# Kernel tuning notes

Measured on AMD Instinct MI355X. Metric: run time of the kernel, lower is better.

## Reference

```python
import jax, jax.numpy as jnp
import numpy as np

NUM_COLS = 8      # MyTopoAgent.num_columns
NUM_SELECTED = 4  # MyTopoAgent.num_selected


def _gatv2(x, src, tgt, Wl, bl, Wr, br, att, bias, n):
    """PyG GATv2Conv (share_weights=False, concat=True, negative_slope=0.2).
    x: [n, Din]; src/tgt: [E] (self loops already appended); att: [H, C]."""
    H, C = att.shape
    xl = (x @ Wl + bl).reshape(n, H, C)   # lin_l(x) -> source transform
    xr = (x @ Wr + br).reshape(n, H, C)   # lin_r(x) -> target transform
    # e_ij = att . leaky_relu(xl[j] + xr[i])  per head
    e = jnp.einsum('ehc,hc->eh', jax.nn.leaky_relu(xl[src] + xr[tgt], 0.2), att)  # [E, H]
    # segment softmax over edges sharing a target node (stable via segment max)
    m = jax.lax.stop_gradient(jax.ops.segment_max(e, tgt, num_segments=n))
    ex = jnp.exp(e - m[tgt])
    denom = jax.ops.segment_sum(ex, tgt, num_segments=n)
    alpha = ex / (denom[tgt] + 1e-16)
    out = jax.ops.segment_sum(xl[src] * alpha[..., None], tgt, num_segments=n)  # [n, H, C]
    return out.reshape(n, H * C) + bias


def setup_inputs() -> dict:
    key = jax.random.key(0)
    B, N, D, Hd, Ch, E = 4, 10000, 128, 128, 7, 640000
    M = B * N
    ks = iter(jax.random.split(key, 40))
    nx = lambda shape: jax.random.normal(next(ks), shape, dtype=jnp.float32) * 0.05
    inp = {}
    inp['x'] = jax.random.normal(next(ks), (B, N, D), dtype=jnp.float32)
    inp['edge_index'] = jax.random.randint(next(ks), (2, E), 0, M)
    inp['gumbel_u'] = jax.random.uniform(next(ks), (B, NUM_COLS, Ch), dtype=jnp.float32,
                                         minval=1e-6, maxval=1.0 - 1e-6)
    # actor gat1(D->Hd), actor gat2(Hd->Ch), critic gat1(D->Hd), critic gat2(Hd->Hd); heads=1
    for pre, di, do in (('a1', D, Hd), ('a2', Hd, Ch), ('c1', D, Hd), ('c2', Hd, Hd)):
        inp[pre + '_Wl'] = nx((di, do))
        inp[pre + '_bl'] = jnp.zeros((do,), jnp.float32)
        inp[pre + '_Wr'] = nx((di, do))
        inp[pre + '_br'] = jnp.zeros((do,), jnp.float32)
        inp[pre + '_att'] = nx((1, do))
        inp[pre + '_b'] = jnp.zeros((do,), jnp.float32)
    inp['fc_W'] = nx((Hd, 1))
    inp['fc_b'] = jnp.zeros((1,), jnp.float32)
    return inp


def reference(x, edge_index, gumbel_u,
              a1_Wl, a1_bl, a1_Wr, a1_br, a1_att, a1_b,
              a2_Wl, a2_bl, a2_Wr, a2_br, a2_att, a2_b,
              c1_Wl, c1_bl, c1_Wr, c1_br, c1_att, c1_b,
              c2_Wl, c2_bl, c2_Wr, c2_br, c2_att, c2_b,
              fc_W, fc_b):
    B, N, D = x.shape
    M = B * N
    xf = x.reshape(M, D)
    loops = jnp.arange(M, dtype=edge_index.dtype)  # PyG add_self_loops
    src = jnp.concatenate([edge_index[0], loops])
    tgt = jnp.concatenate([edge_index[1], loops])
    # ---- actor: GATv2 -> leaky_relu(0.01) -> GATv2 -> softmax ----
    h = _gatv2(xf, src, tgt, a1_Wl, a1_bl, a1_Wr, a1_br, a1_att, a1_b, M)
    h = jax.nn.leaky_relu(h, 0.01)
    logits = _gatv2(h, src, tgt, a2_Wl, a2_bl, a2_Wr, a2_br, a2_att, a2_b, M).reshape(B, N, -1)
    probs = jax.nn.softmax(logits, axis=-1)  # [B, N, 7]
    # multinomial(k=4, no replacement) per column via Gumbel top-k
    g = -jnp.log(-jnp.log(gumbel_u))                       # [B, 8, 7]
    scores = jnp.log(probs[:, :NUM_COLS, :]) + g
    _, action = jax.lax.top_k(scores, NUM_SELECTED)        # [B, 8, 4]
    # torch gather(dim=1): sel[b,i,j] = probs[b, action[b,i,j], j]
    sel = probs[jnp.arange(B)[:, None, None], action, jnp.arange(NUM_SELECTED)[None, None, :]]
    # ---- critic: GATv2 -> leaky_relu(0.01) -> GATv2 -> Linear ----
    hc = _gatv2(xf, src, tgt, c1_Wl, c1_bl, c1_Wr, c1_br, c1_att, c1_b, M)
    hc = jax.nn.leaky_relu(hc, 0.01)
    hc = _gatv2(hc, src, tgt, c2_Wl, c2_bl, c2_Wr, c2_br, c2_att, c2_b, M).reshape(B, N, -1)
    value = hc @ fc_W + fc_b  # [B, N, 1]
    return action, sel, value
```

## Files before the change

kernel.cpp:

```cpp
#include <hip/hip_runtime.h>
#include <math.h>


typedef __attribute__((ext_vector_type(8))) short bf16x8;
typedef __attribute__((ext_vector_type(4))) float f32x4;

__device__ __forceinline__ float wave_reduce_sum(float v){
  #pragma unroll
  for (int o = 32; o > 0; o >>= 1) v += __shfl_xor(v, o);
  return v;
}
__device__ __forceinline__ unsigned short f2bf(float f){
  unsigned int u = __float_as_uint(f);
  u += 0x7FFFu + ((u >> 16) & 1u);
  return (unsigned short)(u >> 16);
}
__device__ __forceinline__ void unpack2(unsigned int u, float& a, float& b){
  a = __uint_as_float(u << 16);
  b = __uint_as_float(u & 0xffff0000u);
}

__global__ void k_scatter(const int* __restrict__ ei, int E,
                          int* __restrict__ cnt, int* __restrict__ bucket,
                          const float* __restrict__ W1l, const float* __restrict__ W1r,
                          const float* __restrict__ W2l, const float* __restrict__ W2r,
                          unsigned short* __restrict__ Wt1, unsigned short* __restrict__ Wt2){
  int e = blockIdx.x * blockDim.x + threadIdx.x;
  if (e < E){
    int s = ei[e], t = ei[E + e];
    int pos = atomicAdd(&cnt[t], 1);
    if (pos < 64) bucket[(size_t)t * 64 + pos] = s;
  } else {
    int r = e - E;
    if (r < 65536){
      int which = r >> 15;
      int lin = r & 32767;
      const float* Wl = which ? W2l : W1l;
      const float* Wr = which ? W2r : W1r;
      unsigned short* Wt = which ? Wt2 : Wt1;
      int n = lin >> 7, k = lin & 127;
      float v = (n < 128) ? Wl[(size_t)k * 128 + n] : Wr[(size_t)k * 128 + (n - 128)];
      Wt[lin] = f2bf(v);
    }
  }
}

__global__ void k_mark1(const int* __restrict__ cnt, const int* __restrict__ bucket,
                        int* __restrict__ flag1, int* __restrict__ list1,
                        int* __restrict__ n1, int N){
  int p = threadIdx.x;
  if (p >= 32) return;
  int node = (p >> 3) * N + (p & 7);
  if (atomicExch(&flag1[node], 1) == 0) list1[atomicAdd(n1, 1)] = node;
  int deg = min(cnt[node], 64);
  const int* crow = bucket + (size_t)node * 64;
  for (int j = 0; j < deg; ++j){
    int s = crow[j];
    if (atomicExch(&flag1[s], 1) == 0) list1[atomicAdd(n1, 1)] = s;
  }
}
__global__ void k_mark2(const int* __restrict__ cnt, const int* __restrict__ bucket,
                        const int* __restrict__ list1, const int* __restrict__ n1,
                        int* __restrict__ flag2, int* __restrict__ list2,
                        int* __restrict__ n2){
  int n = *n1;
  for (int i = blockIdx.x * blockDim.x + threadIdx.x; i < n; i += gridDim.x * blockDim.x){
    int node = list1[i];
    if (atomicExch(&flag2[node], 1) == 0) list2[atomicAdd(n2, 1)] = node;
    int deg = min(cnt[node], 64);
    const int* crow = bucket + (size_t)node * 64;
    for (int j = 0; j < deg; ++j){
      int s = crow[j];
      if (atomicExch(&flag2[s], 1) == 0) list2[atomicAdd(n2, 1)] = s;
    }
  }
}

__device__ __forceinline__ void dev_gemm_dual(
    int bid, const float* __restrict__ A,
    const float* __restrict__ Wl, const float* __restrict__ Wr,
    const float* __restrict__ blv, const float* __restrict__ brv,
    float* __restrict__ XL1, float* __restrict__ XR1,
    const int* __restrict__ list1, const int* __restrict__ list2,
    const int* __restrict__ nn,
    float (*As)[17], float (*Ws)[64]){
  int side = bid >> 7;
  int rem = bid & 127;
  const float* W = side ? Wr : Wl;
  const float* bias = side ? brv : blv;
  float* Out = side ? XR1 : XL1;
  const int* rows = side ? list1 : list2;
  int n = side ? nn[0] : nn[1];
  int tid = threadIdx.x;
  int tx = tid & 15, ty = tid >> 4;
  int colBase = (rem >> 6) * 64;
  int bx = rem & 63;
  int ar = tid >> 2, ac = (tid & 3) << 2;
  int kr = tid >> 4, nc = (tid & 15) << 2;
  for (int base = bx * 64; base < n; base += 64 * 64){
    float acc[4][4] = {};
    int arow = rows[min(base + ar, n - 1)];
    for (int k0 = 0; k0 < 128; k0 += 16){
      float4 av = *(const float4*)(A + (size_t)arow * 128 + k0 + ac);
      As[ar][ac + 0] = av.x; As[ar][ac + 1] = av.y;
      As[ar][ac + 2] = av.z; As[ar][ac + 3] = av.w;
      float4 wv = *(const float4*)(W + (size_t)(k0 + kr) * 128 + colBase + nc);
      *(float4*)&Ws[kr][nc] = wv;
      __syncthreads();
      #pragma unroll
      for (int kk = 0; kk < 16; ++kk){
        float a0 = As[ty * 4 + 0][kk];
        float a1 = As[ty * 4 + 1][kk];
        float a2 = As[ty * 4 + 2][kk];
        float a3 = As[ty * 4 + 3][kk];
        float4 b = *(const float4*)&Ws[kk][tx * 4];
        acc[0][0] += a0 * b.x; acc[0][1] += a0 * b.y; acc[0][2] += a0 * b.z; acc[0][3] += a0 * b.w;
        acc[1][0] += a1 * b.x; acc[1][1] += a1 * b.y; acc[1][2] += a1 * b.z; acc[1][3] += a1 * b.w;
        acc[2][0] += a2 * b.x; acc[2][1] += a2 * b.y; acc[2][2] += a2 * b.z; acc[2][3] += a2 * b.w;
        acc[3][0] += a3 * b.x; acc[3][1] += a3 * b.y; acc[3][2] += a3 * b.z; acc[3][3] += a3 * b.w;
      }
      __syncthreads();
    }
    int cN = colBase + tx * 4;
    float4 bb = *(const float4*)(bias + cN);
    #pragma unroll
    for (int i = 0; i < 4; ++i){
      int r = rows[min(base + ty * 4 + i, n - 1)];
      float4 o;
      o.x = acc[i][0] + bb.x; o.y = acc[i][1] + bb.y;
      o.z = acc[i][2] + bb.z; o.w = acc[i][3] + bb.w;
      *(float4*)(Out + (size_t)r * 128 + cN) = o;
    }
  }
}

template<bool CVT>
__device__ __forceinline__ void dev_gemm_mfma(
    int rblk, const void* __restrict__ Av, const unsigned short* __restrict__ Wt,
    const float* __restrict__ bl, const float* __restrict__ br,
    unsigned short* __restrict__ XL, unsigned short* __restrict__ XR){
  int w = threadIdx.x >> 6, lane = threadIdx.x & 63;
  int l16 = lane & 15, kg = lane >> 4;
  int rBase = rblk * 64 + w * 16;
  f32x4 acc[16];
  #pragma unroll
  for (int i = 0; i < 16; ++i) acc[i] = (f32x4){0.f, 0.f, 0.f, 0.f};
  #pragma unroll
  for (int ks = 0; ks < 4; ++ks){
    bf16x8 a;
    if constexpr (CVT){
      const float* A = (const float*)Av;
      const float* ap = A + (size_t)(rBase + l16) * 128 + ks * 32 + kg * 8;
      float4 f0 = *(const float4*)ap;
      float4 f1 = *(const float4*)(ap + 4);
      union { bf16x8 v; unsigned short s[8]; } u;
      u.s[0] = f2bf(f0.x); u.s[1] = f2bf(f0.y); u.s[2] = f2bf(f0.z); u.s[3] = f2bf(f0.w);
      u.s[4] = f2bf(f1.x); u.s[5] = f2bf(f1.y); u.s[6] = f2bf(f1.z); u.s[7] = f2bf(f1.w);
      a = u.v;
    } else {
      a = *(const bf16x8*)((const unsigned short*)Av + (size_t)(rBase + l16) * 128 + ks * 32 + kg * 8);
    }
    #pragma unroll
    for (int ct = 0; ct < 16; ++ct){
      bf16x8 wv = *(const bf16x8*)(Wt + (size_t)(ct * 16 + l16) * 128 + ks * 32 + kg * 8);
      acc[ct] = __builtin_amdgcn_mfma_f32_16x16x32_bf16(wv, a, acc[ct], 0, 0, 0);
    }
  }
  int row = rBase + l16;
  #pragma unroll
  for (int ct = 0; ct < 16; ++ct){
    int col = ct * 16 + kg * 4;
    const float* bp = (col < 128) ? (bl + col) : (br + (col - 128));
    float4 bb = *(const float4*)bp;
    unsigned int p0 = (unsigned int)f2bf(acc[ct][0] + bb.x) |
                      ((unsigned int)f2bf(acc[ct][1] + bb.y) << 16);
    unsigned int p1 = (unsigned int)f2bf(acc[ct][2] + bb.z) |
                      ((unsigned int)f2bf(acc[ct][3] + bb.w) << 16);
    unsigned short* dst = (col < 128) ? (XL + (size_t)row * 128 + col)
                                      : (XR + (size_t)row * 128 + (col - 128));
    uint2 pk; pk.x = p0; pk.y = p1;
    *(uint2*)dst = pk;
  }
}

template<int MODE>
__device__ __forceinline__ void dev_gather16(
    int gid, int l,
    const unsigned short* __restrict__ XL, const unsigned short* __restrict__ XR,
    const int* __restrict__ cnt, const int* __restrict__ bucket,
    const float* __restrict__ att, const float* __restrict__ bias,
    const float* __restrict__ fcW, const float* __restrict__ fcb,
    void* __restrict__ outp){
  uint4 xu = *(const uint4*)(XR + (size_t)gid * 128 + l * 8);
  float xr[8];
  unpack2(xu.x, xr[0], xr[1]); unpack2(xu.y, xr[2], xr[3]);
  unpack2(xu.z, xr[4], xr[5]); unpack2(xu.w, xr[6], xr[7]);
  float at[8];
  {
    float4 a0 = *(const float4*)(att + l * 8);
    float4 a1 = *(const float4*)(att + l * 8 + 4);
    at[0] = a0.x; at[1] = a0.y; at[2] = a0.z; at[3] = a0.w;
    at[4] = a1.x; at[5] = a1.y; at[6] = a1.z; at[7] = a1.w;
  }
  int deg = min(cnt[gid], 64);
  const int* __restrict__ crow = bucket + (size_t)gid * 64;
  float m = -INFINITY, den = 0.f;
  float acc[8] = {0.f, 0.f, 0.f, 0.f, 0.f, 0.f, 0.f, 0.f};

  auto proc = [&](uint4 u){
    float xl[8];
    unpack2(u.x, xl[0], xl[1]); unpack2(u.y, xl[2], xl[3]);
    unpack2(u.z, xl[4], xl[5]); unpack2(u.w, xl[6], xl[7]);
    float e = 0.f;
    #pragma unroll
    for (int c = 0; c < 8; ++c){
      float v = xl[c] + xr[c];
      v = fmaxf(v, 0.2f * v);
      e = fmaf(v, at[c], e);
    }
    e += __shfl_xor(e, 1, 16);
    e += __shfl_xor(e, 2, 16);
    e += __shfl_xor(e, 4, 16);
    e += __shfl_xor(e, 8, 16);
    if (e > m){
      float sc = __expf(m - e);
      den *= sc;
      #pragma unroll
      for (int c = 0; c < 8; ++c) acc[c] *= sc;
      m = e;
    }
    float p = __expf(e - m);
    den += p;
    #pragma unroll
    for (int c = 0; c < 8; ++c) acc[c] = fmaf(p, xl[c], acc[c]);
  };

  proc(*(const uint4*)(XL + (size_t)gid * 128 + l * 8));

  int nq = deg >> 2;
  int j = 0;
  if (nq > 0){
    uint4 r0, r1, r2, r3;
    {
      int s0 = crow[0], s1 = crow[1], s2 = crow[2], s3 = crow[3];
      r0 = *(const uint4*)(XL + (size_t)s0 * 128 + l * 8);
      r1 = *(const uint4*)(XL + (size_t)s1 * 128 + l * 8);
      r2 = *(const uint4*)(XL + (size_t)s2 * 128 + l * 8);
      r3 = *(const uint4*)(XL + (size_t)s3 * 128 + l * 8);
    }
    for (int q = 1;; ++q){
      bool more = (q < nq);
      uint4 n0, n1, n2, n3;
      if (more){
        int b4 = q * 4;
        int t0 = crow[b4 + 0], t1 = crow[b4 + 1], t2 = crow[b4 + 2], t3 = crow[b4 + 3];
        n0 = *(const uint4*)(XL + (size_t)t0 * 128 + l * 8);
        n1 = *(const uint4*)(XL + (size_t)t1 * 128 + l * 8);
        n2 = *(const uint4*)(XL + (size_t)t2 * 128 + l * 8);
        n3 = *(const uint4*)(XL + (size_t)t3 * 128 + l * 8);
      }
      proc(r0); proc(r1); proc(r2); proc(r3);
      if (!more) break;
      r0 = n0; r1 = n1; r2 = n2; r3 = n3;
    }
    j = nq * 4;
  }
  for (; j < deg; ++j){
    int s = crow[j];
    proc(*(const uint4*)(XL + (size_t)s * 128 + l * 8));
  }

  float r = 1.f / (den + 1e-16f);
  float4 b0 = *(const float4*)(bias + l * 8);
  float4 b1 = *(const float4*)(bias + l * 8 + 4);
  float o[8];
  o[0] = acc[0] * r + b0.x; o[1] = acc[1] * r + b0.y;
  o[2] = acc[2] * r + b0.z; o[3] = acc[3] * r + b0.w;
  o[4] = acc[4] * r + b1.x; o[5] = acc[5] * r + b1.y;
  o[6] = acc[6] * r + b1.z; o[7] = acc[7] * r + b1.w;
  if (MODE == 0){
    #pragma unroll
    for (int c = 0; c < 8; ++c) o[c] = o[c] > 0.f ? o[c] : 0.01f * o[c];
    uint4 pk;
    pk.x = (unsigned int)f2bf(o[0]) | ((unsigned int)f2bf(o[1]) << 16);
    pk.y = (unsigned int)f2bf(o[2]) | ((unsigned int)f2bf(o[3]) << 16);
    pk.z = (unsigned int)f2bf(o[4]) | ((unsigned int)f2bf(o[5]) << 16);
    pk.w = (unsigned int)f2bf(o[6]) | ((unsigned int)f2bf(o[7]) << 16);
    *(uint4*)((unsigned short*)outp + (size_t)gid * 128 + l * 8) = pk;
  } else {
    float4 w0 = *(const float4*)(fcW + l * 8);
    float4 w1 = *(const float4*)(fcW + l * 8 + 4);
    float pv = o[0] * w0.x + o[1] * w0.y + o[2] * w0.z + o[3] * w0.w +
               o[4] * w1.x + o[5] * w1.y + o[6] * w1.z + o[7] * w1.w;
    pv += __shfl_xor(pv, 1, 16);
    pv += __shfl_xor(pv, 2, 16);
    pv += __shfl_xor(pv, 4, 16);
    pv += __shfl_xor(pv, 8, 16);
    if (l == 0) ((float*)outp)[gid] = pv + fcb[0];
  }
}

__device__ __forceinline__ void dev_a1_fused(
    int vbid,
    const float* __restrict__ XL, const float* __restrict__ XR,
    const int* __restrict__ cnt, const int* __restrict__ bucket,
    const float* __restrict__ att, const float* __restrict__ bias,
    const float* __restrict__ Wl7, const float* __restrict__ Wr7,
    const float* __restrict__ bl7, const float* __restrict__ br7,
    float* __restrict__ XL2, float* __restrict__ XR2,
    const int* __restrict__ list, const int* __restrict__ n_dev){
  int n = *n_dev;
  int lane = threadIdx.x & 63;
  const int wstride = (256 * 256) >> 6;
  for (int i = (vbid * 256 + (int)threadIdx.x) >> 6; i < n; i += wstride){
    int wid = list[i];
    float2 xr = ((const float2*)(XR + (size_t)wid * 128))[lane];
    float2 at = ((const float2*)att)[lane];
    int deg = min(cnt[wid], 64);
    const int* crow = bucket + (size_t)wid * 64;
    float m = -INFINITY, den = 0.f, acc0 = 0.f, acc1 = 0.f;
    for (int j = -1; j < deg; ++j){
      int s = (j < 0) ? wid : crow[j];
      float2 xl = ((const float2*)(XL + (size_t)s * 128))[lane];
      float v0 = xl.x + xr.x, v1 = xl.y + xr.y;
      v0 = v0 > 0.f ? v0 : 0.2f * v0;
      v1 = v1 > 0.f ? v1 : 0.2f * v1;
      float e = wave_reduce_sum(v0 * at.x + v1 * at.y);
      float mn = fmaxf(m, e);
      float sc = __expf(m - mn);
      float p  = __expf(e - mn);
      den  = den  * sc + p;
      acc0 = acc0 * sc + p * xl.x;
      acc1 = acc1 * sc + p * xl.y;
      m = mn;
    }
    float r = 1.f / (den + 1e-16f);
    float2 bs = ((const float2*)bias)[lane];
    float o0 = acc0 * r + bs.x;
    float o1 = acc1 * r + bs.y;
    o0 = o0 > 0.f ? o0 : 0.01f * o0;
    o1 = o1 > 0.f ? o1 : 0.01f * o1;
    #pragma unroll
    for (int c = 0; c < 7; ++c){
      float wl0 = Wl7[(size_t)(2 * lane) * 7 + c];
      float wl1 = Wl7[(size_t)(2 * lane + 1) * 7 + c];
      float wr0 = Wr7[(size_t)(2 * lane) * 7 + c];
      float wr1 = Wr7[(size_t)(2 * lane + 1) * 7 + c];
      float dl = wave_reduce_sum(o0 * wl0 + o1 * wl1);
      float dr = wave_reduce_sum(o0 * wr0 + o1 * wr1);
      if (lane == 0){
        XL2[(size_t)wid * 8 + c] = dl + bl7[c];
        XR2[(size_t)wid * 8 + c] = dr + br7[c];
      }
    }
  }
}

__device__ __forceinline__ void dev_a2head(
    float (*pr)[8],
    const float* __restrict__ XL2, const float* __restrict__ XR2,
    const int* __restrict__ cnt, const int* __restrict__ bucket,
    const float* __restrict__ att, const float* __restrict__ bias,
    const float* __restrict__ gu,
    float* __restrict__ out_action, float* __restrict__ out_sel, int N){
  int g = threadIdx.x >> 3, c = threadIdx.x & 7;
  int node = (g >> 3) * N + (g & 7);
  float xr = (c < 7) ? XR2[(size_t)node * 8 + c] : 0.f;
  float at = (c < 7) ? att[c] : 0.f;
  int deg = min(cnt[node], 64);
  const int* crow = bucket + (size_t)node * 64;
  float m = -INFINITY, den = 0.f, acc = 0.f;
  for (int j = -1; j < deg; ++j){
    int s = (j < 0) ? node : crow[j];
    float xl = (c < 7) ? XL2[(size_t)s * 8 + c] : 0.f;
    float v = xl + xr;
    v = fmaxf(v, 0.2f * v);
    float e = v * at;
    e += __shfl_xor(e, 1, 8);
    e += __shfl_xor(e, 2, 8);
    e += __shfl_xor(e, 4, 8);
    if (e > m){
      float sc = __expf(m - e);
      den *= sc; acc *= sc; m = e;
    }
    float p = __expf(e - m);
    den += p;
    acc = fmaf(p, xl, acc);
  }
  float lg = acc / (den + 1e-16f) + ((c < 7) ? bias[c] : 0.f);
  float lgv = (c < 7) ? lg : -INFINITY;
  float mx = lgv;
  mx = fmaxf(mx, __shfl_xor(mx, 1, 8));
  mx = fmaxf(mx, __shfl_xor(mx, 2, 8));
  mx = fmaxf(mx, __shfl_xor(mx, 4, 8));
  float ex = (c < 7) ? expf(lgv - mx) : 0.f;
  float sm = ex;
  sm += __shfl_xor(sm, 1, 8);
  sm += __shfl_xor(sm, 2, 8);
  sm += __shfl_xor(sm, 4, 8);
  pr[g][c] = ex / sm;
  __syncthreads();
  int t = threadIdx.x;
  if (t < 32){
    int b = t >> 3;
    float sc[7];
    #pragma unroll
    for (int cc = 0; cc < 7; ++cc){
      float u = gu[t * 7 + cc];
      float gn = -logf(-logf(u));
      sc[cc] = logf(pr[t][cc]) + gn;
    }
    #pragma unroll
    for (int k = 0; k < 4; ++k){
      float best = -INFINITY; int bi = 0;
      #pragma unroll
      for (int cc = 0; cc < 7; ++cc) if (sc[cc] > best){ best = sc[cc]; bi = cc; }
      sc[bi] = -INFINITY;
      out_action[t * 4 + k] = (float)bi;
      out_sel[t * 4 + k] = pr[b * 8 + bi][k];
    }
  }
}

__global__ __launch_bounds__(256) void k_mega1(
    const float* __restrict__ x,
    const float* __restrict__ a1_Wl, const float* __restrict__ a1_Wr,
    const float* __restrict__ a1_bl, const float* __restrict__ a1_br,
    float* __restrict__ XL1, float* __restrict__ XR1,
    const int* __restrict__ list1, const int* __restrict__ list2,
    const int* __restrict__ nn,
    const unsigned short* __restrict__ Wt1,
    const float* __restrict__ c1_bl, const float* __restrict__ c1_br,
    unsigned short* __restrict__ XLb, unsigned short* __restrict__ XRb){
  __shared__ float As[64][17];
  __shared__ float Ws[16][64];
  int bid = blockIdx.x;
  if (bid < 256){
    dev_gemm_dual(bid, x, a1_Wl, a1_Wr, a1_bl, a1_br, XL1, XR1, list1, list2, nn, As, Ws);
  } else {
    dev_gemm_mfma<true>(bid - 256, x, Wt1, c1_bl, c1_br, XLb, XRb);
  }
}

__global__ __launch_bounds__(256) void k_mega2(
    const unsigned short* __restrict__ XLb, const unsigned short* __restrict__ XRb,
    const int* __restrict__ cnt, const int* __restrict__ bucket,
    const float* __restrict__ c1_att, const float* __restrict__ c1_b,
    unsigned short* __restrict__ Hb, int M, int G0,
    const float* __restrict__ XL1, const float* __restrict__ XR1,
    const float* __restrict__ a1_att, const float* __restrict__ a1_b,
    const float* __restrict__ Wl7, const float* __restrict__ Wr7,
    const float* __restrict__ bl7, const float* __restrict__ br7,
    float* __restrict__ XL2, float* __restrict__ XR2,
    const int* __restrict__ list1, const int* __restrict__ n1){
  int bid = blockIdx.x;
  if (bid < G0){
    int gid = (bid * 256 + (int)threadIdx.x) >> 4;
    int l = threadIdx.x & 15;
    if (gid < M)
      dev_gather16<0>(gid, l, XLb, XRb, cnt, bucket, c1_att, c1_b,
                      nullptr, nullptr, (void*)Hb);
  } else {
    dev_a1_fused(bid - G0, XL1, XR1, cnt, bucket, a1_att, a1_b,
                 Wl7, Wr7, bl7, br7, XL2, XR2, list1, n1);
  }
}

__global__ __launch_bounds__(256) void k_mega3(
    const unsigned short* __restrict__ Hb, const unsigned short* __restrict__ Wt2,
    const float* __restrict__ c2_bl, const float* __restrict__ c2_br,
    unsigned short* __restrict__ XLb, unsigned short* __restrict__ XRb, int nMfma,
    const float* __restrict__ XL2, const float* __restrict__ XR2,
    const int* __restrict__ cnt, const int* __restrict__ bucket,
    const float* __restrict__ a2_att, const float* __restrict__ a2_b,
    const float* __restrict__ gu,
    float* __restrict__ out_action, float* __restrict__ out_sel, int N){
  __shared__ float pr[32][8];
  int bid = blockIdx.x;
  if (bid < nMfma){
    dev_gemm_mfma<false>(bid, Hb, Wt2, c2_bl, c2_br, XLb, XRb);
  } else {
    dev_a2head(pr, XL2, XR2, cnt, bucket, a2_att, a2_b, gu, out_action, out_sel, N);
  }
}

__global__ __launch_bounds__(256) void k_gather_v(
    const unsigned short* __restrict__ XLb, const unsigned short* __restrict__ XRb,
    const int* __restrict__ cnt, const int* __restrict__ bucket,
    const float* __restrict__ att, const float* __restrict__ bias,
    const float* __restrict__ fcW, const float* __restrict__ fcb,
    float* __restrict__ out_value, int M){
  int gid = (blockIdx.x * blockDim.x + threadIdx.x) >> 4;
  int l = threadIdx.x & 15;
  if (gid < M)
    dev_gather16<1>(gid, l, XLb, XRb, cnt, bucket, att, bias, fcW, fcb, (void*)out_value);
}

extern "C" void kernel_launch(void* const* d_in, const int* in_sizes, int n_in,
                              void* d_out, int out_size, void* d_ws, size_t ws_size,
                              hipStream_t stream){
  const float* x  = (const float*)d_in[0];
  const int*   ei = (const int*)d_in[1];
  const float* gu = (const float*)d_in[2];
  const float* a1_Wl = (const float*)d_in[3],  *a1_bl = (const float*)d_in[4];
  const float* a1_Wr = (const float*)d_in[5],  *a1_br = (const float*)d_in[6];
  const float* a1_att= (const float*)d_in[7],  *a1_b  = (const float*)d_in[8];
  const float* a2_Wl = (const float*)d_in[9],  *a2_bl = (const float*)d_in[10];
  const float* a2_Wr = (const float*)d_in[11], *a2_br = (const float*)d_in[12];
  const float* a2_att= (const float*)d_in[13], *a2_b  = (const float*)d_in[14];
  const float* c1_Wl = (const float*)d_in[15], *c1_bl = (const float*)d_in[16];
  const float* c1_Wr = (const float*)d_in[17], *c1_br = (const float*)d_in[18];
  const float* c1_att= (const float*)d_in[19], *c1_b  = (const float*)d_in[20];
  const float* c2_Wl = (const float*)d_in[21], *c2_bl = (const float*)d_in[22];
  const float* c2_Wr = (const float*)d_in[23], *c2_br = (const float*)d_in[24];
  const float* c2_att= (const float*)d_in[25], *c2_b  = (const float*)d_in[26];
  const float* fc_W  = (const float*)d_in[27], *fc_b  = (const float*)d_in[28];

  const int M = in_sizes[0] / 128;
  const int E = in_sizes[1] / 2;
  const int B = in_sizes[2] / 56;
  const int N = M / B;
  const int nw = B * 8;
  const int T = 256;

  char* ws = (char*)d_ws;
  size_t off = 0;
  auto alloc = [&](size_t bytes) -> void* {
    void* p = ws + off;
    off += (bytes + 255) & ~(size_t)255;
    return p;
  };
  int*   cnt    = (int*)alloc((size_t)(3 * M + 2) * 4);
  int*   flag1  = cnt + M;
  int*   flag2  = flag1 + M;
  int*   nn     = flag2 + M;
  int*   bucket = (int*)alloc((size_t)M * 64 * 4);
  int*   list1  = (int*)alloc((size_t)M * 4);
  int*   list2  = (int*)alloc((size_t)M * 4);
  float* XL2    = (float*)alloc((size_t)M * 8 * 4);
  float* XR2    = (float*)alloc((size_t)M * 8 * 4);
  unsigned short* Wt1 = (unsigned short*)alloc((size_t)256 * 128 * 2);
  unsigned short* Wt2 = (unsigned short*)alloc((size_t)256 * 128 * 2);
  float* XL1 = (float*)alloc((size_t)M * 128 * 4);
  float* XR1 = (float*)alloc((size_t)M * 128 * 4);
  unsigned short* XLb = (unsigned short*)alloc((size_t)M * 128 * 2);
  unsigned short* XRb = (unsigned short*)alloc((size_t)M * 128 * 2);
  unsigned short* Hb  = (unsigned short*)alloc((size_t)M * 128 * 2);
  (void)ws_size; (void)n_in; (void)out_size;

  float* out_action = (float*)d_out;
  float* out_sel    = out_action + (size_t)nw * 4;
  float* out_value  = out_sel + (size_t)nw * 4;

  const int G0 = (M * 16 + T - 1) / T;
  const int nMfma = M / 64;

  hipMemsetAsync(cnt, 0, (size_t)(3 * M + 2) * 4, stream);
  k_scatter<<<(E + 65536 + T - 1) / T, T, 0, stream>>>(ei, E, cnt, bucket,
      c1_Wl, c1_Wr, c2_Wl, c2_Wr, Wt1, Wt2);

  k_mark1<<<1, 64, 0, stream>>>(cnt, bucket, flag1, list1, &nn[0], N);
  k_mark2<<<64, T, 0, stream>>>(cnt, bucket, list1, &nn[0], flag2, list2, &nn[1]);

  k_mega1<<<256 + nMfma, T, 0, stream>>>(x, a1_Wl, a1_Wr, a1_bl, a1_br,
      XL1, XR1, list1, list2, nn, Wt1, c1_bl, c1_br, XLb, XRb);

  k_mega2<<<G0 + 256, T, 0, stream>>>(XLb, XRb, cnt, bucket, c1_att, c1_b,
      Hb, M, G0, XL1, XR1, a1_att, a1_b, a2_Wl, a2_Wr, a2_bl, a2_br,
      XL2, XR2, list1, &nn[0]);

  k_mega3<<<nMfma + 1, T, 0, stream>>>(Hb, Wt2, c2_bl, c2_br, XLb, XRb, nMfma,
      XL2, XR2, cnt, bucket, a2_att, a2_b, gu, out_action, out_sel, N);

  k_gather_v<<<G0, T, 0, stream>>>(XLb, XRb, cnt, bucket, c2_att, c2_b,
      fc_W, fc_b, out_value, M);
}
```

Measured before the change: 248.8 us.

## Rebalance actor GEMM blocks, schedule critical blocks first, replace memset with kernel

The actor layer-1 dual GEMM gets more blocks in total, and they are split unevenly: 384 go to the larger list2 row set (lin_l) and 128 to list1 (lin_r), so the larger side gets more parallelism. In the second mega kernel the dependency-heavy a1_fused blocks now take the lowest block indices so they are dispatched before the many gather blocks. The hipMemsetAsync is replaced with a small zeroing kernel, which may lower launch or memset overhead. Each change shifts load balance or scheduling order and can cost extra block overhead.

Result: faster. 241.9 us (-2.8%).

```diff
diff --git a/kernel.cpp b/kernel.cpp
--- a/kernel.cpp
+++ b/kernel.cpp
@@ -18,6 +18,11 @@
 __device__ __forceinline__ void unpack2(unsigned int u, float& a, float& b){
   a = __uint_as_float(u << 16);
   b = __uint_as_float(u & 0xffff0000u);
+}
+
+__global__ void k_zero(int* __restrict__ p, int n){
+  int i = blockIdx.x * blockDim.x + threadIdx.x;
+  if (i < n) p[i] = 0;
 }
 
 __global__ void k_scatter(const int* __restrict__ ei, int E,
@@ -84,20 +89,21 @@
     const int* __restrict__ list1, const int* __restrict__ list2,
     const int* __restrict__ nn,
     float (*As)[17], float (*Ws)[64]){
-  int side = bid >> 7;
-  int rem = bid & 127;
-  const float* W = side ? Wr : Wl;
-  const float* bias = side ? brv : blv;
-  float* Out = side ? XR1 : XL1;
-  const int* rows = side ? list1 : list2;
-  int n = side ? nn[0] : nn[1];
+  const float* W; const float* bias; float* Out; const int* rows; int n;
+  int colBase, bx, nbx;
+  if (bid < 384){
+    W = Wl; bias = blv; Out = XL1; rows = list2; n = nn[1];
+    colBase = (bid / 192) * 64; bx = bid % 192; nbx = 192;
+  } else {
+    int rem = bid - 384;
+    W = Wr; bias = brv; Out = XR1; rows = list1; n = nn[0];
+    colBase = (rem / 64) * 64; bx = rem % 64; nbx = 64;
+  }
   int tid = threadIdx.x;
   int tx = tid & 15, ty = tid >> 4;
-  int colBase = (rem >> 6) * 64;
-  int bx = rem & 63;
   int ar = tid >> 2, ac = (tid & 3) << 2;
   int kr = tid >> 4, nc = (tid & 15) << 2;
-  for (int base = bx * 64; base < n; base += 64 * 64){
+  for (int base = bx * 64; base < n; base += nbx * 64){
     float acc[4][4] = {};
     int arow = rows[min(base + ar, n - 1)];
     for (int k0 = 0; k0 < 128; k0 += 16){
@@ -435,10 +441,10 @@
   __shared__ float As[64][17];
   __shared__ float Ws[16][64];
   int bid = blockIdx.x;
-  if (bid < 256){
+  if (bid < 512){
     dev_gemm_dual(bid, x, a1_Wl, a1_Wr, a1_bl, a1_br, XL1, XR1, list1, list2, nn, As, Ws);
   } else {
-    dev_gemm_mfma<true>(bid - 256, x, Wt1, c1_bl, c1_br, XLb, XRb);
+    dev_gemm_mfma<true>(bid - 512, x, Wt1, c1_bl, c1_br, XLb, XRb);
   }
 }
 
@@ -454,15 +460,16 @@
     float* __restrict__ XL2, float* __restrict__ XR2,
     const int* __restrict__ list1, const int* __restrict__ n1){
   int bid = blockIdx.x;
-  if (bid < G0){
-    int gid = (bid * 256 + (int)threadIdx.x) >> 4;
+  if (bid < 256){
+    dev_a1_fused(bid, XL1, XR1, cnt, bucket, a1_att, a1_b,
+                 Wl7, Wr7, bl7, br7, XL2, XR2, list1, n1);
+  } else {
+    int gbid = bid - 256;
+    int gid = (gbid * 256 + (int)threadIdx.x) >> 4;
     int l = threadIdx.x & 15;
     if (gid < M)
       dev_gather16<0>(gid, l, XLb, XRb, cnt, bucket, c1_att, c1_b,
                       nullptr, nullptr, (void*)Hb);
-  } else {
-    dev_a1_fused(bid - G0, XL1, XR1, cnt, bucket, a1_att, a1_b,
-                 Wl7, Wr7, bl7, br7, XL2, XR2, list1, n1);
   }
 }
 
@@ -554,18 +561,19 @@
 
   const int G0 = (M * 16 + T - 1) / T;
   const int nMfma = M / 64;
-
-  hipMemsetAsync(cnt, 0, (size_t)(3 * M + 2) * 4, stream);
+  const int nz = 3 * M + 2;
+
+  k_zero<<<(nz + T - 1) / T, T, 0, stream>>>(cnt, nz);
   k_scatter<<<(E + 65536 + T - 1) / T, T, 0, stream>>>(ei, E, cnt, bucket,
       c1_Wl, c1_Wr, c2_Wl, c2_Wr, Wt1, Wt2);
 
   k_mark1<<<1, 64, 0, stream>>>(cnt, bucket, flag1, list1, &nn[0], N);
   k_mark2<<<64, T, 0, stream>>>(cnt, bucket, list1, &nn[0], flag2, list2, &nn[1]);
 
-  k_mega1<<<256 + nMfma, T, 0, stream>>>(x, a1_Wl, a1_Wr, a1_bl, a1_br,
+  k_mega1<<<512 + nMfma, T, 0, stream>>>(x, a1_Wl, a1_Wr, a1_bl, a1_br,
       XL1, XR1, list1, list2, nn, Wt1, c1_bl, c1_br, XLb, XRb);
 
-  k_mega2<<<G0 + 256, T, 0, stream>>>(XLb, XRb, cnt, bucket, c1_att, c1_b,
+  k_mega2<<<256 + G0, T, 0, stream>>>(XLb, XRb, cnt, bucket, c1_att, c1_b,
       Hb, M, G0, XL1, XR1, a1_att, a1_b, a2_Wl, a2_Wr, a2_bl, a2_br,
       XL2, XR2, list1, &nn[0]);
 
```
